# Performance work log

Measured on AMD Instinct MI355X. Metric: run time of the kernel, lower is better.

## Reference

```python
import jax, jax.numpy as jnp
import numpy as np

N_NODES = 10000
N_EDGES = 160000
F = 128
NRB = 32


def setup_inputs() -> dict:
    key = jax.random.key(0)
    ks = jax.random.split(key, 20)
    inp = {
        "s": jax.random.normal(ks[0], (N_NODES, F), jnp.float32),
        "v": jax.random.normal(ks[1], (N_NODES, 3, F), jnp.float32),
        "radial_embeddings_1": jax.random.normal(ks[2], (N_EDGES, NRB), jnp.float32),
        "radial_embeddings_2": jax.random.normal(ks[3], (N_EDGES, NRB), jnp.float32),
        "radial_embeddings_3": jax.random.normal(ks[4], (N_EDGES, NRB), jnp.float32),
        "f_cut_1": jax.random.uniform(ks[5], (N_EDGES,), jnp.float32),
        "f_cut_2": jax.random.uniform(ks[6], (N_EDGES,), jnp.float32),
        "f_cut_3": jax.random.uniform(ks[7], (N_EDGES,), jnp.float32),
        "unit_vectors_1": jax.random.normal(ks[8], (N_EDGES, 3), jnp.float32),
        "unit_vectors_2": jax.random.normal(ks[9], (N_EDGES, 3), jnp.float32),
        "unit_vectors_3": jax.random.normal(ks[10], (N_EDGES, 3), jnp.float32),
        "edge_index": jax.random.randint(ks[11], (2, N_EDGES), 0, N_NODES, jnp.int64),
    }
    # parameters (Linear uses y = x @ W.T + b; we store transposed for x @ W)
    sc1 = 1.0 / np.sqrt(F)
    sc2 = 1.0 / np.sqrt(NRB)
    inp["W1"] = jax.random.uniform(ks[12], (F, F), jnp.float32, -sc1, sc1)
    inp["b1"] = jax.random.uniform(ks[13], (F,), jnp.float32, -sc1, sc1)
    inp["W2"] = jax.random.uniform(ks[14], (F, 8 * F), jnp.float32, -sc1, sc1)
    inp["b2"] = jax.random.uniform(ks[15], (8 * F,), jnp.float32, -sc1, sc1)
    inp["Wr"] = jax.random.uniform(ks[16], (NRB, 8 * F), jnp.float32, -sc2, sc2)
    inp["br"] = jax.random.uniform(ks[17], (8 * F,), jnp.float32, -sc2, sc2)
    return inp


def reference(s, v, radial_embeddings_1, radial_embeddings_2, radial_embeddings_3,
              f_cut_1, f_cut_2, f_cut_3,
              unit_vectors_1, unit_vectors_2, unit_vectors_3,
              edge_index, W1, b1, W2, b2, Wr, br):
    idx_i, idx_j = edge_index[0], edge_index[1]
    n_nodes = s.shape[0]
    nf = W1.shape[0]

    # phi = Linear(F,F) -> SiLU -> Linear(F,8F)   [N, 8F]
    phi = jax.nn.silu(s @ W1 + b1) @ W2 + b2

    # shared-weight radial filter over 3 branches  [E, 8F]
    W = ((radial_embeddings_1 @ Wr + br) * f_cut_1[:, None]
         + (radial_embeddings_2 @ Wr + br) * f_cut_2[:, None]
         + (radial_embeddings_3 @ Wr + br) * f_cut_3[:, None])

    x = phi[idx_j] * W                                    # [E, 8F]
    x_s, x_vv, x_vs1, x_vs2, x_vs3, x_vc1, x_vc2, x_vc3 = jnp.split(x, 8, axis=-1)

    ds = jax.ops.segment_sum(x_s, idx_i, num_segments=n_nodes)

    vj = v[idx_j]                                         # [E, 3, F]
    ex = lambda a: a[:, None, :]                          # [E,1,F] broadcast over xyz
    cr = lambda u: jnp.cross(vj, u[..., None], axis=1)    # [E, 3, F]

    x_v = (vj * ex(x_vv)
           + ex(x_vs1) * unit_vectors_1[..., None]
           + ex(x_vs2) * unit_vectors_2[..., None]
           + ex(x_vs3) * unit_vectors_3[..., None]
           + ex(x_vc1) * cr(unit_vectors_1)
           + ex(x_vc2) * cr(unit_vectors_2)
           + ex(x_vc3) * cr(unit_vectors_3))              # [E, 3, F]

    dv = jax.ops.segment_sum(x_v, idx_i, num_segments=n_nodes)
    return (s + ds, v + dv)
```

## Files before the change

kernel.cpp:

```cpp
#include <hip/hip_runtime.h>

#define N_NODES 10000
#define N_EDGES 160000
#define MAXT     20000
#define MSG_GRID 5000

typedef __attribute__((ext_vector_type(8))) __bf16 bf16x8;
typedef __attribute__((ext_vector_type(8))) unsigned short u16x8;
typedef __attribute__((ext_vector_type(4))) float f32x4;

static __device__ __forceinline__ unsigned short f2bf(float x) {
    union { float f; unsigned u; } un;
    un.f = x;
    unsigned r = un.u + 0x7fffu + ((un.u >> 16) & 1u);
    return (unsigned short)(r >> 16);
}

static __device__ __forceinline__ float bf2f(unsigned short h) {
    union { unsigned u; float f; } un;
    un.u = ((unsigned)h) << 16;
    return un.f;
}

__global__ __launch_bounds__(256) void init_kernel(
    const float* __restrict__ s, const float* __restrict__ v,
    const int* __restrict__ eix,
    const float* __restrict__ W1, const float* __restrict__ W2,
    const float* __restrict__ Wr,
    float* __restrict__ out0, float* __restrict__ out1,
    unsigned short* __restrict__ vbf2, int* __restrict__ cnt,
    unsigned short* __restrict__ W1T, unsigned short* __restrict__ W2T,
    unsigned short* __restrict__ WrT)
{
    int tid = blockIdx.x * 256 + threadIdx.x;
    if (tid < N_NODES * 384) out1[tid] = v[tid];
    if (tid < N_NODES * 128) {
        out0[tid] = s[tid];
        int n = tid >> 7, f = tid & 127;
        ushort4 q;
        q.x = f2bf(v[(size_t)n * 384 + f]);
        q.y = f2bf(v[(size_t)n * 384 + 128 + f]);
        q.z = f2bf(v[(size_t)n * 384 + 256 + f]);
        q.w = 0;
        *reinterpret_cast<ushort4*>(vbf2 + (size_t)tid * 4) = q;
    }
    if (tid < 131072) {
        int n = tid >> 7, k = tid & 127;
        W2T[tid] = f2bf(W2[k * 1024 + n]);
    }
    if (tid < 16384) {
        int n = tid >> 7, k = tid & 127;
        W1T[tid] = f2bf(W1[k * 128 + n]);
    }
    if (tid < 32768) {
        int n = tid >> 5, k = tid & 31;
        WrT[tid] = f2bf(Wr[k * 1024 + n]);
    }
    if (tid < N_EDGES) atomicAdd(&cnt[eix[tid]], 1);
}

__global__ __launch_bounds__(1024) void scan_kernel(
    const int* __restrict__ cnt, int* __restrict__ cursor,
    int* __restrict__ tile_node, int* __restrict__ tile_e0,
    int* __restrict__ tile_cnt, int* __restrict__ ntiles)
{
    __shared__ int ws0[16], ws1[16];
    __shared__ int run0_s, run1_s;
    int t = threadIdx.x, lane = t & 63, wid = t >> 6;
    if (t == 0) { run0_s = 0; run1_s = 0; }
    __syncthreads();
    for (int base = 0; base < N_NODES; base += 1024) {
        int idx = base + t;
        int deg = (idx < N_NODES) ? cnt[idx] : 0;
        int tc = (deg + 15) >> 4;
        int x0 = deg, x1 = tc;
        #pragma unroll
        for (int o = 1; o < 64; o <<= 1) {
            int y0 = __shfl_up(x0, o), y1 = __shfl_up(x1, o);
            if (lane >= o) { x0 += y0; x1 += y1; }
        }
        if (lane == 63) { ws0[wid] = x0; ws1[wid] = x1; }
        __syncthreads();
        if (wid == 0) {
            int w0 = (lane < 16) ? ws0[lane] : 0;
            int w1 = (lane < 16) ? ws1[lane] : 0;
            #pragma unroll
            for (int o = 1; o < 16; o <<= 1) {
                int y0 = __shfl_up(w0, o), y1 = __shfl_up(w1, o);
                if (lane >= o) { w0 += y0; w1 += y1; }
            }
            if (lane < 16) { ws0[lane] = w0; ws1[lane] = w1; }
        }
        __syncthreads();
        int wb0 = wid ? ws0[wid - 1] : 0;
        int wb1 = wid ? ws1[wid - 1] : 0;
        int ex0 = run0_s + wb0 + x0 - deg;
        int ex1 = run1_s + wb1 + x1 - tc;
        if (idx < N_NODES) {
            cursor[idx] = ex0;
            for (int k = 0; k < tc; ++k) {
                tile_node[ex1 + k] = idx;
                tile_e0[ex1 + k]   = ex0 + k * 16;
                int rem = deg - k * 16;
                tile_cnt[ex1 + k]  = rem < 16 ? rem : 16;
            }
        }
        __syncthreads();
        if (t == 0) { run0_s += ws0[15]; run1_s += ws1[15]; }
        __syncthreads();
    }
    if (t == 0) *ntiles = run1_s;
}

__global__ __launch_bounds__(256) void rc_kernel(
    const float* __restrict__ R1, const float* __restrict__ R2,
    const float* __restrict__ R3,
    const float* __restrict__ f1, const float* __restrict__ f2,
    const float* __restrict__ f3,
    const int* __restrict__ eix, int* __restrict__ cursor,
    unsigned short* __restrict__ Rc, float* __restrict__ fsum,
    int* __restrict__ elist)
{
    int tid = blockIdx.x * 256 + threadIdx.x;
    int e = tid >> 3, sub = tid & 7;
    if (e >= N_EDGES) return;
    float a = f1[e], b = f2[e], c = f3[e];
    int k0 = sub * 4;
    float4 r1 = *reinterpret_cast<const float4*>(R1 + (size_t)e * 32 + k0);
    float4 r2 = *reinterpret_cast<const float4*>(R2 + (size_t)e * 32 + k0);
    float4 r3 = *reinterpret_cast<const float4*>(R3 + (size_t)e * 32 + k0);
    ushort4 o;
    o.x = f2bf(r1.x * a + r2.x * b + r3.x * c);
    o.y = f2bf(r1.y * a + r2.y * b + r3.y * c);
    o.z = f2bf(r1.z * a + r2.z * b + r3.z * c);
    o.w = f2bf(r1.w * a + r2.w * b + r3.w * c);
    *reinterpret_cast<ushort4*>(Rc + (size_t)e * 32 + k0) = o;
    if (sub == 0) {
        fsum[e] = a + b + c;
        int slot = atomicAdd(&cursor[eix[e]], 1);
        elist[slot] = e;
    }
}

__global__ __launch_bounds__(256) void phi_kernel(
    const float* __restrict__ s, const unsigned short* __restrict__ W1T,
    const float* __restrict__ b1, const unsigned short* __restrict__ W2T,
    const float* __restrict__ b2, unsigned short* __restrict__ phi2)
{
    __shared__ unsigned short h_lds[64][136];
    int t = threadIdx.x, lane = t & 63, w = t >> 6;
    int quad = lane >> 4, l16 = lane & 15;
    int m0 = (blockIdx.x >> 2) * 64;
    int colg = blockIdx.x & 3;

    int arow = m0 + w * 16 + l16;
    if (arow > N_NODES - 1) arow = N_NODES - 1;
    bf16x8 afr[4];
    #pragma unroll
    for (int ks = 0; ks < 4; ++ks) {
        const float* sp = s + (size_t)arow * 128 + ks * 32 + quad * 8;
        #pragma unroll
        for (int jj = 0; jj < 8; ++jj) afr[ks][jj] = (__bf16)sp[jj];
    }
    #pragma unroll
    for (int cg = 0; cg < 8; ++cg) {
        int col = cg * 16 + l16;
        f32x4 acc = {0.f, 0.f, 0.f, 0.f};
        #pragma unroll
        for (int ks = 0; ks < 4; ++ks) {
            bf16x8 bf = *reinterpret_cast<const bf16x8*>(W1T + (size_t)col * 128 + ks * 32 + quad * 8);
            acc = __builtin_amdgcn_mfma_f32_16x16x32_bf16(afr[ks], bf, acc, 0, 0, 0);
        }
        float bb = b1[col];
        #pragma unroll
        for (int r = 0; r < 4; ++r) {
            int row = w * 16 + quad * 4 + r;
            float val = acc[r] + bb;
            h_lds[row][col] = f2bf(val / (1.f + __expf(-val)));
        }
    }
    __syncthreads();

    bf16x8 a2[4][4];
    #pragma unroll
    for (int rg = 0; rg < 4; ++rg)
        #pragma unroll
        for (int ks = 0; ks < 4; ++ks)
            a2[rg][ks] = *reinterpret_cast<const bf16x8*>(&h_lds[rg * 16 + l16][ks * 32 + quad * 8]);
    #pragma unroll
    for (int i = 0; i < 4; ++i) {
        int col = colg * 256 + w * 64 + i * 16 + l16;
        f32x4 acc2[4] = {{0,0,0,0},{0,0,0,0},{0,0,0,0},{0,0,0,0}};
        #pragma unroll
        for (int ks = 0; ks < 4; ++ks) {
            bf16x8 bf = *reinterpret_cast<const bf16x8*>(W2T + (size_t)col * 128 + ks * 32 + quad * 8);
            #pragma unroll
            for (int rg = 0; rg < 4; ++rg)
                acc2[rg] = __builtin_amdgcn_mfma_f32_16x16x32_bf16(a2[rg][ks], bf, acc2[rg], 0, 0, 0);
        }
        float bb = b2[col];
        int f = col & 127, cc = col >> 7;
        #pragma unroll
        for (int rg = 0; rg < 4; ++rg)
            #pragma unroll
            for (int r = 0; r < 4; ++r) {
                int row = m0 + rg * 16 + quad * 4 + r;
                if (row < N_NODES)
                    phi2[(size_t)row * 1024 + f * 8 + cc] = f2bf(acc2[rg][r] + bb);
            }
    }
}

__global__ __launch_bounds__(512) void msg_kernel(
    const unsigned short* __restrict__ Rc, const float* __restrict__ fsum,
    const int* __restrict__ eix,
    const unsigned short* __restrict__ phi2, const unsigned short* __restrict__ vbf2,
    const unsigned short* __restrict__ WrT, const float* __restrict__ br,
    const int* __restrict__ elist,
    const int* __restrict__ tile_node, const int* __restrict__ tile_e0,
    const int* __restrict__ tile_cnt, const int* __restrict__ ntiles,
    const float* __restrict__ u1, const float* __restrict__ u2,
    const float* __restrict__ u3,
    float* __restrict__ out0, float* __restrict__ out1)
{
    int t = threadIdx.x, lane = t & 63, w = t >> 6;
    int quad = lane >> 4, l16 = lane & 15;
    int fcol = w * 16 + l16;
    const int nt = *ntiles;
    const int* idx_j = eix + N_EDGES;

    bf16x8 bfrag[8];
    float brv[8];
    #pragma unroll
    for (int c = 0; c < 8; ++c) {
        int col = c * 128 + fcol;
        bfrag[c] = *reinterpret_cast<const bf16x8*>(WrT + (size_t)col * 32 + quad * 8);
        brv[c] = br[col];
    }

    __shared__ float srow[2][16][12];

    for (int t4 = 0; t4 < 4; ++t4) {
        int tile = blockIdx.x + t4 * MSG_GRID;
        if (tile >= nt) break;
        int node = tile_node[tile], e0 = tile_e0[tile], tcnt = tile_cnt[tile];
        int p = t4 & 1;

        if (t < 192) {
            int row = t / 12, c = t - row * 12;
            float val = 0.f;
            if (row < tcnt) {
                int eid = elist[e0 + row];
                if (c == 0)      val = __int_as_float(idx_j[eid]);
                else if (c == 1) val = fsum[eid];
                else if (c < 5)  val = u1[(size_t)eid * 3 + c - 2];
                else if (c < 8)  val = u2[(size_t)eid * 3 + c - 5];
                else if (c < 11) val = u3[(size_t)eid * 3 + c - 8];
            }
            srow[p][row][c] = val;
        }

        int er = e0 + (l16 < tcnt ? l16 : 0);
        int eid_a = elist[er];
        bf16x8 af;
        if (l16 < tcnt)
            af = *reinterpret_cast<const bf16x8*>(Rc + (size_t)eid_a * 32 + quad * 8);
        else {
            #pragma unroll
            for (int q = 0; q < 8; ++q) af[q] = (__bf16)0.f;
        }

        f32x4 acc[8];
        #pragma unroll
        for (int c = 0; c < 8; ++c) {
            f32x4 z = {0.f, 0.f, 0.f, 0.f};
            acc[c] = __builtin_amdgcn_mfma_f32_16x16x32_bf16(af, bfrag[c], z, 0, 0, 0);
        }

        __syncthreads();

        float ds = 0.f, d0 = 0.f, d1 = 0.f, d2 = 0.f;
        #pragma unroll
        for (int r = 0; r < 4; ++r) {
            int row = quad * 4 + r;
            int j = __float_as_int(srow[p][row][0]);
            float fs = srow[p][row][1];
            u16x8 ph = *reinterpret_cast<const u16x8*>(phi2 + ((size_t)j * 128 + fcol) * 8);
            ushort4 vb = *reinterpret_cast<const ushort4*>(vbf2 + ((size_t)j * 128 + fcol) * 4);
            float x[8];
            #pragma unroll
            for (int c = 0; c < 8; ++c)
                x[c] = bf2f(ph[c]) * (acc[c][r] + brv[c] * fs);
            float vjx = bf2f(vb.x), vjy = bf2f(vb.y), vjz = bf2f(vb.z);
            float u1x = srow[p][row][2], u1y = srow[p][row][3], u1z = srow[p][row][4];
            float u2x = srow[p][row][5], u2y = srow[p][row][6], u2z = srow[p][row][7];
            float u3x = srow[p][row][8], u3y = srow[p][row][9], u3z = srow[p][row][10];

            ds += x[0];
            d0 += vjx * x[1] + u1x * x[2] + u2x * x[3] + u3x * x[4]
                + x[5] * (vjy * u1z - vjz * u1y)
                + x[6] * (vjy * u2z - vjz * u2y)
                + x[7] * (vjy * u3z - vjz * u3y);
            d1 += vjy * x[1] + u1y * x[2] + u2y * x[3] + u3y * x[4]
                + x[5] * (vjz * u1x - vjx * u1z)
                + x[6] * (vjz * u2x - vjx * u2z)
                + x[7] * (vjz * u3x - vjx * u3z);
            d2 += vjz * x[1] + u1z * x[2] + u2z * x[3] + u3z * x[4]
                + x[5] * (vjx * u1y - vjy * u1x)
                + x[6] * (vjx * u2y - vjy * u2x)
                + x[7] * (vjx * u3y - vjy * u3x);
        }

        ds += __shfl_xor(ds, 16); ds += __shfl_xor(ds, 32);
        d0 += __shfl_xor(d0, 16); d0 += __shfl_xor(d0, 32);
        d1 += __shfl_xor(d1, 16); d1 += __shfl_xor(d1, 32);
        d2 += __shfl_xor(d2, 16); d2 += __shfl_xor(d2, 32);

        if (quad == 0) {
            atomicAdd(&out0[(size_t)node * 128 + fcol], ds);
            size_t vo = (size_t)node * 384 + fcol;
            atomicAdd(&out1[vo], d0);
            atomicAdd(&out1[vo + 128], d1);
            atomicAdd(&out1[vo + 256], d2);
        }
    }
}

extern "C" void kernel_launch(void* const* d_in, const int* in_sizes, int n_in,
                              void* d_out, int out_size, void* d_ws, size_t ws_size,
                              hipStream_t stream) {
    const float* s  = (const float*)d_in[0];
    const float* v  = (const float*)d_in[1];
    const float* R1 = (const float*)d_in[2];
    const float* R2 = (const float*)d_in[3];
    const float* R3 = (const float*)d_in[4];
    const float* f1 = (const float*)d_in[5];
    const float* f2 = (const float*)d_in[6];
    const float* f3 = (const float*)d_in[7];
    const float* u1 = (const float*)d_in[8];
    const float* u2 = (const float*)d_in[9];
    const float* u3 = (const float*)d_in[10];
    const int*  eix = (const int*)d_in[11];
    const float* W1 = (const float*)d_in[12];
    const float* b1 = (const float*)d_in[13];
    const float* W2 = (const float*)d_in[14];
    const float* b2 = (const float*)d_in[15];
    const float* Wr = (const float*)d_in[16];
    const float* br = (const float*)d_in[17];

    char* ws = (char*)d_ws;
    size_t off = 0;
    auto alloc = [&](size_t bytes) -> void* {
        void* p = ws + off;
        off = (off + bytes + 255) & ~(size_t)255;
        return p;
    };
    int* cnt       = (int*)alloc((size_t)N_NODES * 4);
    int* cursor    = (int*)alloc((size_t)N_NODES * 4);
    int* tile_node = (int*)alloc((size_t)MAXT * 4);
    int* tile_e0   = (int*)alloc((size_t)MAXT * 4);
    int* tile_cnt  = (int*)alloc((size_t)MAXT * 4);
    int* ntiles    = (int*)alloc(4);
    int* elist     = (int*)alloc((size_t)N_EDGES * 4);
    unsigned short* Rc   = (unsigned short*)alloc((size_t)N_EDGES * 32 * 2);
    float* fsum          = (float*)alloc((size_t)N_EDGES * 4);
    unsigned short* vbf2 = (unsigned short*)alloc((size_t)N_NODES * 128 * 4 * 2);
    unsigned short* phi2 = (unsigned short*)alloc((size_t)N_NODES * 1024 * 2);
    unsigned short* W1T  = (unsigned short*)alloc(128 * 128 * 2);
    unsigned short* W2T  = (unsigned short*)alloc(1024 * 128 * 2);
    unsigned short* WrT  = (unsigned short*)alloc(1024 * 32 * 2);
    (void)ws_size; (void)in_sizes; (void)n_in; (void)out_size;

    float* out0 = (float*)d_out;
    float* out1 = out0 + (size_t)N_NODES * 128;

    hipMemsetAsync(cnt, 0, (size_t)N_NODES * 4, stream);
    init_kernel<<<15000, 256, 0, stream>>>(s, v, eix, W1, W2, Wr,
                                           out0, out1, vbf2, cnt, W1T, W2T, WrT);
    scan_kernel<<<1, 1024, 0, stream>>>(cnt, cursor, tile_node, tile_e0, tile_cnt, ntiles);
    rc_kernel<<<5000, 256, 0, stream>>>(R1, R2, R3, f1, f2, f3, eix, cursor,
                                        Rc, fsum, elist);
    phi_kernel<<<628, 256, 0, stream>>>(s, W1T, b1, W2T, b2, phi2);
    msg_kernel<<<MSG_GRID, 512, 0, stream>>>(Rc, fsum, eix, phi2, vbf2, WrT, br,
                                             elist, tile_node, tile_e0, tile_cnt,
                                             ntiles, u1, u2, u3, out0, out1);
}
```

Before: 365.1 us.

## Scatter edge data into padded per-node tile slots, removing elist indirection in msg kernel

The rc kernel now writes the combined radial rows and a 16-float header (idx_j, fsum, three unit vectors) straight into tile-aligned slots ordered by destination node. A separate pad section zero-fills the unused slots in each node's last tile. The msg kernel can then read tile rows contiguously, with no elist lookup, no LDS staging and no __syncthreads. The cross-product terms are also refactored algebraically into one cross product with a combined vector q. The cost is a larger workspace (about 20% more slots, plus 64-byte headers) and MAXT is tightened, which assumes the tile count stays under that bound.

New measurement: 440.9 us. 20.8% more time.

```diff
diff --git a/kernel.cpp b/kernel.cpp
--- a/kernel.cpp
+++ b/kernel.cpp
@@ -2,8 +2,11 @@
 
 #define N_NODES 10000
 #define N_EDGES 160000
-#define MAXT     20000
+#define MAXT     19400
+#define NSLOT    (MAXT * 16 + 16)
 #define MSG_GRID 5000
+#define RC_BLOCKS 5000
+#define PAD_BLOCKS 625
 
 typedef __attribute__((ext_vector_type(8))) __bf16 bf16x8;
 typedef __attribute__((ext_vector_type(8))) unsigned short u16x8;
@@ -61,69 +64,79 @@
 
 __global__ __launch_bounds__(1024) void scan_kernel(
     const int* __restrict__ cnt, int* __restrict__ cursor,
-    int* __restrict__ tile_node, int* __restrict__ tile_e0,
-    int* __restrict__ tile_cnt, int* __restrict__ ntiles)
-{
-    __shared__ int ws0[16], ws1[16];
-    __shared__ int run0_s, run1_s;
+    int* __restrict__ nb, int* __restrict__ tile_node,
+    int* __restrict__ ntiles)
+{
+    __shared__ int ws[16];
+    __shared__ int run_s;
     int t = threadIdx.x, lane = t & 63, wid = t >> 6;
-    if (t == 0) { run0_s = 0; run1_s = 0; }
+    if (t == 0) run_s = 0;
     __syncthreads();
     for (int base = 0; base < N_NODES; base += 1024) {
         int idx = base + t;
         int deg = (idx < N_NODES) ? cnt[idx] : 0;
         int tc = (deg + 15) >> 4;
-        int x0 = deg, x1 = tc;
+        int x = tc;
         #pragma unroll
         for (int o = 1; o < 64; o <<= 1) {
-            int y0 = __shfl_up(x0, o), y1 = __shfl_up(x1, o);
-            if (lane >= o) { x0 += y0; x1 += y1; }
-        }
-        if (lane == 63) { ws0[wid] = x0; ws1[wid] = x1; }
+            int y = __shfl_up(x, o);
+            if (lane >= o) x += y;
+        }
+        if (lane == 63) ws[wid] = x;
         __syncthreads();
         if (wid == 0) {
-            int w0 = (lane < 16) ? ws0[lane] : 0;
-            int w1 = (lane < 16) ? ws1[lane] : 0;
+            int wv = (lane < 16) ? ws[lane] : 0;
             #pragma unroll
             for (int o = 1; o < 16; o <<= 1) {
-                int y0 = __shfl_up(w0, o), y1 = __shfl_up(w1, o);
-                if (lane >= o) { w0 += y0; w1 += y1; }
+                int y = __shfl_up(wv, o);
+                if (lane >= o) wv += y;
             }
-            if (lane < 16) { ws0[lane] = w0; ws1[lane] = w1; }
+            if (lane < 16) ws[lane] = wv;
         }
         __syncthreads();
-        int wb0 = wid ? ws0[wid - 1] : 0;
-        int wb1 = wid ? ws1[wid - 1] : 0;
-        int ex0 = run0_s + wb0 + x0 - deg;
-        int ex1 = run1_s + wb1 + x1 - tc;
+        int wb = wid ? ws[wid - 1] : 0;
+        int ex = run_s + wb + x - tc;
         if (idx < N_NODES) {
-            cursor[idx] = ex0;
-            for (int k = 0; k < tc; ++k) {
-                tile_node[ex1 + k] = idx;
-                tile_e0[ex1 + k]   = ex0 + k * 16;
-                int rem = deg - k * 16;
-                tile_cnt[ex1 + k]  = rem < 16 ? rem : 16;
-            }
+            nb[idx] = ex * 16;
+            cursor[idx] = ex * 16;
+            for (int k = 0; k < tc; ++k) tile_node[ex + k] = idx;
         }
         __syncthreads();
-        if (t == 0) { run0_s += ws0[15]; run1_s += ws1[15]; }
+        if (t == 0) run_s += ws[15];
         __syncthreads();
     }
-    if (t == 0) *ntiles = run1_s;
-}
-
-__global__ __launch_bounds__(256) void rc_kernel(
+    if (t == 0) *ntiles = run_s;
+}
+
+__global__ __launch_bounds__(256) void rc_pad_kernel(
     const float* __restrict__ R1, const float* __restrict__ R2,
     const float* __restrict__ R3,
     const float* __restrict__ f1, const float* __restrict__ f2,
     const float* __restrict__ f3,
-    const int* __restrict__ eix, int* __restrict__ cursor,
-    unsigned short* __restrict__ Rc, float* __restrict__ fsum,
-    int* __restrict__ elist)
-{
+    const float* __restrict__ u1, const float* __restrict__ u2,
+    const float* __restrict__ u3,
+    const int* __restrict__ eix, const int* __restrict__ cnt,
+    const int* __restrict__ nb, int* __restrict__ cursor,
+    unsigned short* __restrict__ Rc_s, float* __restrict__ hdr)
+{
+    if (blockIdx.x >= RC_BLOCKS) {
+        int t2 = (blockIdx.x - RC_BLOCKS) * 256 + threadIdx.x;
+        int n = t2 >> 4, r = t2 & 15;
+        int deg = cnt[n], tc = (deg + 15) >> 4;
+        int p = deg + r;
+        if (p < tc * 16) {
+            size_t slot = (size_t)nb[n] + p;
+            f32x4 z = {0.f, 0.f, 0.f, 0.f};
+            f32x4* hp = reinterpret_cast<f32x4*>(hdr + slot * 16);
+            hp[0] = z; hp[1] = z; hp[2] = z; hp[3] = z;
+            f32x4* rp = reinterpret_cast<f32x4*>(Rc_s + slot * 32);
+            rp[0] = z; rp[1] = z; rp[2] = z; rp[3] = z;
+        }
+        return;
+    }
     int tid = blockIdx.x * 256 + threadIdx.x;
     int e = tid >> 3, sub = tid & 7;
-    if (e >= N_EDGES) return;
+    int lane = threadIdx.x & 63;
     float a = f1[e], b = f2[e], c = f3[e];
     int k0 = sub * 4;
     float4 r1 = *reinterpret_cast<const float4*>(R1 + (size_t)e * 32 + k0);
@@ -134,11 +147,21 @@
     o.y = f2bf(r1.y * a + r2.y * b + r3.y * c);
     o.z = f2bf(r1.z * a + r2.z * b + r3.z * c);
     o.w = f2bf(r1.w * a + r2.w * b + r3.w * c);
-    *reinterpret_cast<ushort4*>(Rc + (size_t)e * 32 + k0) = o;
+    int slot = 0;
+    if (sub == 0) slot = atomicAdd(&cursor[eix[e]], 1);
+    slot = __shfl(slot, lane & 56);
+    *reinterpret_cast<ushort4*>(Rc_s + (size_t)slot * 32 + k0) = o;
     if (sub == 0) {
-        fsum[e] = a + b + c;
-        int slot = atomicAdd(&cursor[eix[e]], 1);
-        elist[slot] = e;
+        float4 h;
+        h.x = __int_as_float(eix[N_EDGES + e]);
+        h.y = a + b + c;
+        h.z = 0.f; h.w = 0.f;
+        *reinterpret_cast<float4*>(hdr + (size_t)slot * 16) = h;
+    } else if (sub < 4) {
+        const float* up = (sub == 1 ? u1 : (sub == 2 ? u2 : u3)) + (size_t)e * 3;
+        float4 h;
+        h.x = up[0]; h.y = up[1]; h.z = up[2]; h.w = 0.f;
+        *reinterpret_cast<float4*>(hdr + (size_t)slot * 16 + (size_t)sub * 4) = h;
     }
 }
 
@@ -212,22 +235,16 @@
 }
 
 __global__ __launch_bounds__(512) void msg_kernel(
-    const unsigned short* __restrict__ Rc, const float* __restrict__ fsum,
-    const int* __restrict__ eix,
+    const unsigned short* __restrict__ Rc_s, const float* __restrict__ hdr,
     const unsigned short* __restrict__ phi2, const unsigned short* __restrict__ vbf2,
     const unsigned short* __restrict__ WrT, const float* __restrict__ br,
-    const int* __restrict__ elist,
-    const int* __restrict__ tile_node, const int* __restrict__ tile_e0,
-    const int* __restrict__ tile_cnt, const int* __restrict__ ntiles,
-    const float* __restrict__ u1, const float* __restrict__ u2,
-    const float* __restrict__ u3,
+    const int* __restrict__ tile_node, const int* __restrict__ ntiles,
     float* __restrict__ out0, float* __restrict__ out1)
 {
     int t = threadIdx.x, lane = t & 63, w = t >> 6;
     int quad = lane >> 4, l16 = lane & 15;
     int fcol = w * 16 + l16;
     const int nt = *ntiles;
-    const int* idx_j = eix + N_EDGES;
 
     bf16x8 bfrag[8];
     float brv[8];
@@ -238,38 +255,13 @@
         brv[c] = br[col];
     }
 
-    __shared__ float srow[2][16][12];
-
     for (int t4 = 0; t4 < 4; ++t4) {
         int tile = blockIdx.x + t4 * MSG_GRID;
         if (tile >= nt) break;
-        int node = tile_node[tile], e0 = tile_e0[tile], tcnt = tile_cnt[tile];
-        int p = t4 & 1;
-
-        if (t < 192) {
-            int row = t / 12, c = t - row * 12;
-            float val = 0.f;
-            if (row < tcnt) {
-                int eid = elist[e0 + row];
-                if (c == 0)      val = __int_as_float(idx_j[eid]);
-                else if (c == 1) val = fsum[eid];
-                else if (c < 5)  val = u1[(size_t)eid * 3 + c - 2];
-                else if (c < 8)  val = u2[(size_t)eid * 3 + c - 5];
-                else if (c < 11) val = u3[(size_t)eid * 3 + c - 8];
-            }
-            srow[p][row][c] = val;
-        }
-
-        int er = e0 + (l16 < tcnt ? l16 : 0);
-        int eid_a = elist[er];
-        bf16x8 af;
-        if (l16 < tcnt)
-            af = *reinterpret_cast<const bf16x8*>(Rc + (size_t)eid_a * 32 + quad * 8);
-        else {
-            #pragma unroll
-            for (int q = 0; q < 8; ++q) af[q] = (__bf16)0.f;
-        }
-
+        int node = tile_node[tile];
+        size_t s0 = (size_t)tile * 16;
+
+        bf16x8 af = *reinterpret_cast<const bf16x8*>(Rc_s + (s0 + l16) * 32 + quad * 8);
         f32x4 acc[8];
         #pragma unroll
         for (int c = 0; c < 8; ++c) {
@@ -277,38 +269,37 @@
             acc[c] = __builtin_amdgcn_mfma_f32_16x16x32_bf16(af, bfrag[c], z, 0, 0, 0);
         }
 
-        __syncthreads();
+        int jj[4]; float fsv[4];
+        #pragma unroll
+        for (int r = 0; r < 4; ++r) {
+            size_t slot = s0 + (quad * 4 + r);
+            float2 h0 = *reinterpret_cast<const float2*>(hdr + slot * 16);
+            jj[r] = __float_as_int(h0.x);
+            fsv[r] = h0.y;
+        }
 
         float ds = 0.f, d0 = 0.f, d1 = 0.f, d2 = 0.f;
         #pragma unroll
         for (int r = 0; r < 4; ++r) {
-            int row = quad * 4 + r;
-            int j = __float_as_int(srow[p][row][0]);
-            float fs = srow[p][row][1];
-            u16x8 ph = *reinterpret_cast<const u16x8*>(phi2 + ((size_t)j * 128 + fcol) * 8);
-            ushort4 vb = *reinterpret_cast<const ushort4*>(vbf2 + ((size_t)j * 128 + fcol) * 4);
+            size_t slot = s0 + (quad * 4 + r);
+            const f32x4* hp = reinterpret_cast<const f32x4*>(hdr + slot * 16);
+            size_t o = (size_t)jj[r] * 128 + fcol;
+            u16x8 ph = *reinterpret_cast<const u16x8*>(phi2 + o * 8);
+            ushort4 vb = *reinterpret_cast<const ushort4*>(vbf2 + o * 4);
+            f32x4 U1 = hp[1], U2 = hp[2], U3 = hp[3];
+            float fs = fsv[r];
             float x[8];
             #pragma unroll
             for (int c = 0; c < 8; ++c)
                 x[c] = bf2f(ph[c]) * (acc[c][r] + brv[c] * fs);
             float vjx = bf2f(vb.x), vjy = bf2f(vb.y), vjz = bf2f(vb.z);
-            float u1x = srow[p][row][2], u1y = srow[p][row][3], u1z = srow[p][row][4];
-            float u2x = srow[p][row][5], u2y = srow[p][row][6], u2z = srow[p][row][7];
-            float u3x = srow[p][row][8], u3y = srow[p][row][9], u3z = srow[p][row][10];
-
+            float qx = x[5] * U1.x + x[6] * U2.x + x[7] * U3.x;
+            float qy = x[5] * U1.y + x[6] * U2.y + x[7] * U3.y;
+            float qz = x[5] * U1.z + x[6] * U2.z + x[7] * U3.z;
             ds += x[0];
-            d0 += vjx * x[1] + u1x * x[2] + u2x * x[3] + u3x * x[4]
-                + x[5] * (vjy * u1z - vjz * u1y)
-                + x[6] * (vjy * u2z - vjz * u2y)
-                + x[7] * (vjy * u3z - vjz * u3y);
-            d1 += vjy * x[1] + u1y * x[2] + u2y * x[3] + u3y * x[4]
-                + x[5] * (vjz * u1x - vjx * u1z)
-                + x[6] * (vjz * u2x - vjx * u2z)
-                + x[7] * (vjz * u3x - vjx * u3z);
-            d2 += vjz * x[1] + u1z * x[2] + u2z * x[3] + u3z * x[4]
-                + x[5] * (vjx * u1y - vjy * u1x)
-                + x[6] * (vjx * u2y - vjy * u2x)
-                + x[7] * (vjx * u3y - vjy * u3x);
+            d0 += x[1] * vjx + x[2] * U1.x + x[3] * U2.x + x[4] * U3.x + vjy * qz - vjz * qy;
+            d1 += x[1] * vjy + x[2] * U1.y + x[3] * U2.y + x[4] * U3.y + vjz * qx - vjx * qz;
+            d2 += x[1] * vjz + x[2] * U1.z + x[3] * U2.z + x[4] * U3.z + vjx * qy - vjy * qx;
         }
 
         ds += __shfl_xor(ds, 16); ds += __shfl_xor(ds, 32);
@@ -357,13 +348,11 @@
     };
     int* cnt       = (int*)alloc((size_t)N_NODES * 4);
     int* cursor    = (int*)alloc((size_t)N_NODES * 4);
+    int* nb        = (int*)alloc((size_t)N_NODES * 4);
     int* tile_node = (int*)alloc((size_t)MAXT * 4);
-    int* tile_e0   = (int*)alloc((size_t)MAXT * 4);
-    int* tile_cnt  = (int*)alloc((size_t)MAXT * 4);
     int* ntiles    = (int*)alloc(4);
-    int* elist     = (int*)alloc((size_t)N_EDGES * 4);
-    unsigned short* Rc   = (unsigned short*)alloc((size_t)N_EDGES * 32 * 2);
-    float* fsum          = (float*)alloc((size_t)N_EDGES * 4);
+    unsigned short* Rc_s = (unsigned short*)alloc((size_t)NSLOT * 32 * 2);
+    float* hdr           = (float*)alloc((size_t)NSLOT * 16 * 4);
     unsigned short* vbf2 = (unsigned short*)alloc((size_t)N_NODES * 128 * 4 * 2);
     unsigned short* phi2 = (unsigned short*)alloc((size_t)N_NODES * 1024 * 2);
     unsigned short* W1T  = (unsigned short*)alloc(128 * 128 * 2);
@@ -377,11 +366,10 @@
     hipMemsetAsync(cnt, 0, (size_t)N_NODES * 4, stream);
     init_kernel<<<15000, 256, 0, stream>>>(s, v, eix, W1, W2, Wr,
                                            out0, out1, vbf2, cnt, W1T, W2T, WrT);
-    scan_kernel<<<1, 1024, 0, stream>>>(cnt, cursor, tile_node, tile_e0, tile_cnt, ntiles);
-    rc_kernel<<<5000, 256, 0, stream>>>(R1, R2, R3, f1, f2, f3, eix, cursor,
-                                        Rc, fsum, elist);
+    scan_kernel<<<1, 1024, 0, stream>>>(cnt, cursor, nb, tile_node, ntiles);
+    rc_pad_kernel<<<RC_BLOCKS + PAD_BLOCKS, 256, 0, stream>>>(
+        R1, R2, R3, f1, f2, f3, u1, u2, u3, eix, cnt, nb, cursor, Rc_s, hdr);
     phi_kernel<<<628, 256, 0, stream>>>(s, W1T, b1, W2T, b2, phi2);
-    msg_kernel<<<MSG_GRID, 512, 0, stream>>>(Rc, fsum, eix, phi2, vbf2, WrT, br,
-                                             elist, tile_node, tile_e0, tile_cnt,
-                                             ntiles, u1, u2, u3, out0, out1);
-}
+    msg_kernel<<<MSG_GRID, 512, 0, stream>>>(Rc_s, hdr, phi2, vbf2, WrT, br,
+                                             tile_node, ntiles, out0, out1);
+}
```
